# Optimization experiments

Measured on AMD Instinct MI355X. Metric: run time of the kernel, lower is better.

Reference implementation:

```python
import jax, jax.numpy as jnp
import numpy as np

N, E, B = 10000, 160000, 16
IN, H, A, L, OUT = 16, 64, 8, 2, 1
MSG_IN = 2 * (H + 1) + 1   # 131 = concat(x_i, x_j, additional_message_features)
UPD_IN = H + 1 + H         # 129 = concat(x_aug, aggregated message)


def _tp(h, a, W, b):
    # scalar-irreps fully-connected O3 tensor product == bilinear map + bias
    return jnp.einsum('ni,nj,ijk->nk', h, a, W) + b


def setup_inputs() -> dict:
    key = jax.random.key(0)
    ks = jax.random.split(key, 24)
    f32 = jnp.float32
    def rn(k, shape, scale=1.0):
        return jax.random.normal(k, shape, f32) * scale
    def w(k, shape):
        fan = shape[-3] * shape[-2]
        return rn(k, shape, 1.0 / np.sqrt(fan))
    return {
        'x': rn(ks[0], (N, IN)),
        'edge_index': jax.random.randint(ks[1], (2, E), 0, N),
        'edge_attr': rn(ks[2], (E, A)),
        'node_attr': rn(ks[3], (N, A)),
        'additional_message_features': rn(ks[4], (E, 1)),
        'additional_node_features': rn(ks[5], (N, 1)),
        'batch': jnp.sort(jax.random.randint(ks[6], (N,), 0, B)),
        'W_emb': w(ks[7], (IN + 1, A, H)), 'b_emb': jnp.zeros((H,), f32),
        'Wm1': w(ks[8], (L, MSG_IN, A, H)), 'bm1': jnp.zeros((L, H), f32),
        'Wm2': w(ks[9], (L, H, A, H)), 'bm2': jnp.zeros((L, H), f32),
        'Wu1': w(ks[10], (L, UPD_IN, A, H)), 'bu1': jnp.zeros((L, H), f32),
        'Wu2': w(ks[11], (L, H, A, H)), 'bu2': jnp.zeros((L, H), f32),
        'Wp1': w(ks[12], (H, A, H)), 'bp1': jnp.zeros((H,), f32),
        'Wp2': w(ks[13], (H, A, H)), 'bp2': jnp.zeros((H,), f32),
        'Wq1': rn(ks[14], (H, H), 1.0 / np.sqrt(H)), 'bq1': jnp.zeros((H,), f32),
        'Wq2': rn(ks[15], (H, OUT), 1.0 / np.sqrt(H)), 'bq2': jnp.zeros((OUT,), f32),
    }


def _forward(x, edge_attr, node_attr, amf, anf,
             W_emb, b_emb, Wm1, bm1, Wm2, bm2, Wu1, bu1, Wu2, bu2,
             Wp1, bp1, Wp2, bp2, Wq1, bq1, Wq2, bq2, edge_index, batch):
    silu = jax.nn.silu
    src, dst = edge_index[0], edge_index[1]  # source_to_target: aggregate at dst
    n = x.shape[0]
    # embedding: concat additional node features, bilinear TP with node_attr
    h = _tp(jnp.concatenate([x, anf], -1), node_attr, W_emb, b_emb)          # [N,H]
    for l in range(Wm1.shape[0]):  # loop over structurally distinct layers
        h_aug = jnp.concatenate([h, anf], -1)                                # [N,H+1]
        m_in = jnp.concatenate([h_aug[dst], h_aug[src], amf], -1)            # [E,MSG_IN]
        m = silu(_tp(m_in, edge_attr, Wm1[l], bm1[l]))                       # TP + swish gate
        m = silu(_tp(m, edge_attr, Wm2[l], bm2[l]))                          # sg2=True -> gated too
        agg = jax.ops.segment_sum(m, dst, num_segments=n)                    # scatter-add [N,H]
        u = silu(_tp(jnp.concatenate([h_aug, agg], -1), node_attr, Wu1[l], bu1[l]))
        u = _tp(u, node_attr, Wu2[l], bu2[l])                                # no gate on 2nd TP
        h = h + u                                                            # residual, adnid stripped
    # pre-pool MLP (SwishGate TP then plain TP)
    p = silu(_tp(h, node_attr, Wp1, bp1))
    p = _tp(p, node_attr, Wp2, bp2)                                          # [N,POOL=H]
    # global mean pool over graphs
    counts = jax.ops.segment_sum(jnp.ones((n,), p.dtype), batch, num_segments=B)
    g = jax.ops.segment_sum(p, batch, num_segments=B) / jnp.maximum(counts, 1.0)[:, None]
    # post-pool: TP with trivial 1x0e attr == plain linear
    g = silu(g @ Wq1 + bq1)
    return g @ Wq2 + bq2                                                     # [B,OUT]


def reference(x, edge_index, edge_attr, node_attr, additional_message_features,
              additional_node_features, batch, W_emb, b_emb, Wm1, bm1, Wm2, bm2,
              Wu1, bu1, Wu2, bu2, Wp1, bp1, Wp2, bp2, Wq1, bq1, Wq2, bq2):
    return _forward(x, edge_attr, node_attr, additional_message_features,
                    additional_node_features, W_emb, b_emb, Wm1, bm1, Wm2, bm2,
                    Wu1, bu1, Wu2, bu2, Wp1, bp1, Wp2, bp2, Wq1, bq1, Wq2, bq2,
                    edge_index, batch)
```

## Files before the change

kernel.cpp:

```cpp
#include <hip/hip_runtime.h>
#include <hip/hip_bf16.h>
#include <math.h>

constexpr int N = 10000;
constexpr int E = 160000;
constexpr int B = 16;
constexpr int POOL_CHUNKS = 80;
constexpr int MS = 72;
constexpr int HS = 96;

typedef short bf16x8 __attribute__((ext_vector_type(8)));
typedef short bf16x4 __attribute__((ext_vector_type(4)));
typedef float f32x4 __attribute__((ext_vector_type(4)));

__device__ __forceinline__ float silu_f(float x) {
    return x / (1.0f + __expf(-x));
}
__device__ __forceinline__ float bf2f(short s) {
    union { unsigned u; float f; } c; c.u = (unsigned)(unsigned short)s << 16; return c.f;
}

__global__ __launch_bounds__(256) void k_w2(
        const float* __restrict__ Wsrc,
        __hip_bfloat16* __restrict__ Whi, __hip_bfloat16* __restrict__ Wlo) {
    int idx = blockIdx.x * 256 + threadIdx.x;
    int l = idx >> 15;
    int rem = idx & 32767;
    int kk = rem >> 11;
    int nt = (rem >> 9) & 3;
    int c  = (rem >> 5) & 15;
    int q  = (rem >> 3) & 3;
    int j  = rem & 7;
    int i = q * 16 + kk;
    int k = nt * 16 + c;
    float wv = Wsrc[(size_t)l * 32768 + i * 512 + j * 64 + k];
    __hip_bfloat16 hi = __float2bfloat16(wv);
    Whi[idx] = hi;
    Wlo[idx] = __float2bfloat16(wv - __bfloat162float(hi));
}

__global__ __launch_bounds__(256) void k_w2h(
        const float* __restrict__ Wsrc, __hip_bfloat16* __restrict__ Whi) {
    int idx = blockIdx.x * 256 + threadIdx.x;
    int l = idx >> 15;
    int rem = idx & 32767;
    int kk = rem >> 11;
    int nt = (rem >> 9) & 3;
    int c  = (rem >> 5) & 15;
    int q  = (rem >> 3) & 3;
    int j  = rem & 7;
    int i = q * 16 + kk;
    int k = nt * 16 + c;
    Whi[idx] = __float2bfloat16(Wsrc[(size_t)l * 32768 + i * 512 + j * 64 + k]);
}

__global__ __launch_bounds__(256) void k_wu1(
        const float* __restrict__ Wu1,
        __hip_bfloat16* __restrict__ Whi, __hip_bfloat16* __restrict__ Wlo) {
    int idx = blockIdx.x * 256 + threadIdx.x;
    int l = idx / 67584;
    int rem = idx % 67584;
    int kk = rem / 2048;
    int r2 = rem % 2048;
    int nt = (r2 >> 9) & 3;
    int c  = (r2 >> 5) & 15;
    int q  = (r2 >> 3) & 3;
    int j  = r2 & 7;
    int i = q * 33 + kk;
    float wv = (i < 129) ? Wu1[(size_t)l * 129 * 512 + i * 512 + j * 64 + nt * 16 + c] : 0.f;
    __hip_bfloat16 hi = __float2bfloat16(wv);
    Whi[idx] = hi;
    Wlo[idx] = __float2bfloat16(wv - __bfloat162float(hi));
}

__global__ __launch_bounds__(256) void k_wm1z(
        const float* __restrict__ Wm1, __hip_bfloat16* __restrict__ Whi) {
    int idx = blockIdx.x * 256 + threadIdx.x;
    int l = idx / 71680;
    int rem = idx % 71680;
    int kkn = rem >> 9;
    int off = rem & 511;
    int kk = kkn >> 2;
    int nt = kkn & 3;
    int c16 = off >> 5;
    int q = (off >> 3) & 3;
    int j = off & 7;
    int k = nt * 16 + c16;
    int wi = -1;
    if (kk < 17) { int i = q * 17 + kk; if (i <= 64) wi = i; }
    else if (kk < 34) { int s = q * 17 + (kk - 17); if (s <= 64) wi = 65 + s; }
    else { if (q == 0) wi = 130; }
    float wv = (wi >= 0) ? Wm1[((size_t)l * 131 + wi) * 512 + j * 64 + k] : 0.f;
    Whi[idx] = __float2bfloat16(wv);
}

__device__ __forceinline__ void zgemm_stage(
        const __hip_bfloat16* xsrc, int xstride, int kkmax, int Lq,
        int w, int c16, int q, int lofs, const float* naA,
        const __hip_bfloat16* __restrict__ Whi, const __hip_bfloat16* __restrict__ Wlo,
        float (*part_s)[16][64]) {
    f32x4 zero4 = {0.f, 0.f, 0.f, 0.f};
    f32x4 acc[4];
#pragma unroll
    for (int nt = 0; nt < 4; ++nt) acc[nt] = zero4;
    for (int kk = w; kk < kkmax; kk += 4) {
        bf16x8 bh[4], bl[4];
#pragma unroll
        for (int nt = 0; nt < 4; ++nt) {
            int off = (kk * 4 + nt) * 512 + lofs;
            bh[nt] = *(const bf16x8*)(Whi + off);
            bl[nt] = *(const bf16x8*)(Wlo + off);
        }
        float mv = __bfloat162float(xsrc[c16 * xstride + q * Lq + kk]);
        union { bf16x8 v; __hip_bfloat16 hx[8]; } au;
#pragma unroll
        for (int j = 0; j < 8; ++j) au.hx[j] = __float2bfloat16(mv * naA[j]);
#pragma unroll
        for (int nt = 0; nt < 4; ++nt) {
            acc[nt] = __builtin_amdgcn_mfma_f32_16x16x32_bf16(au.v, bh[nt], acc[nt], 0, 0, 0);
            acc[nt] = __builtin_amdgcn_mfma_f32_16x16x32_bf16(au.v, bl[nt], acc[nt], 0, 0, 0);
        }
    }
#pragma unroll
    for (int nt = 0; nt < 4; ++nt)
#pragma unroll
        for (int r = 0; r < 4; ++r) part_s[w][q * 4 + r][nt * 16 + c16] = acc[nt][r];
}

__global__ __launch_bounds__(256) void k_embed_hb(
        const float* __restrict__ x, const float* __restrict__ anf,
        const float* __restrict__ na, const float* __restrict__ W_emb,
        const float* __restrict__ b_emb,
        float* __restrict__ h, __hip_bfloat16* __restrict__ hb, float* __restrict__ agg) {
    __shared__ float xs[16][18];
    __shared__ float na_s[16][8];
    int tid = threadIdx.x, w = tid >> 6, l = tid & 63;
    int n0 = blockIdx.x * 16;
    {
        int r = tid >> 4, c = tid & 15;
        xs[r][c] = x[(size_t)(n0 + r) * 16 + c];
    }
    if (tid < 16) xs[tid][16] = anf[n0 + tid];
    if (tid < 128) na_s[tid >> 3][tid & 7] = na[(size_t)n0 * 8 + tid];
    float4 z4 = {0.f, 0.f, 0.f, 0.f};
    ((float4*)(agg + (size_t)blockIdx.x * 1024))[tid] = z4;
    for (int t = tid; t < 192; t += 256)
        ((float4*)(hb + (size_t)n0 * HS))[t] = z4;
    __syncthreads();
    float acc[4];
#pragma unroll
    for (int t = 0; t < 4; ++t) acc[t] = b_emb[l];
    for (int i = 0; i < 17; ++i) {
#pragma unroll
        for (int j = 0; j < 8; ++j) {
            float wv = W_emb[(i * 8 + j) * 64 + l];
#pragma unroll
            for (int t = 0; t < 4; ++t) {
                int nn = w * 4 + t;
                acc[t] = fmaf(xs[nn][i] * na_s[nn][j], wv, acc[t]);
            }
        }
    }
    int slot = (l / 17) * 24 + l % 17;
#pragma unroll
    for (int t = 0; t < 4; ++t) {
        int n = n0 + w * 4 + t;
        h[(size_t)n * 64 + l] = acc[t];
        hb[(size_t)n * HS + slot] = __float2bfloat16(acc[t]);
    }
    if (tid < 16) hb[(size_t)(n0 + tid) * HS + 85] = __float2bfloat16(xs[tid][16]);
}

__global__ __launch_bounds__(256, 4) void k_edge(
        const int* __restrict__ eidx, const float* __restrict__ ea,
        const float* __restrict__ amf, const __hip_bfloat16* __restrict__ hb,
        const __hip_bfloat16* __restrict__ W1hi, const float* __restrict__ bm1_l,
        const __hip_bfloat16* __restrict__ W2hi,
        const float* __restrict__ bm2_l, float* __restrict__ agg) {
    __shared__ __align__(16) __hip_bfloat16 m_s[128 * MS];
    __shared__ float ea_s[128][9];
    __shared__ float amf_s[128];
    __shared__ int src_s[128], dst_s[128];
    __shared__ float bm1_s[64], bm2_s[64];
    int tid = threadIdx.x;
    int l = tid & 63, w = tid >> 6;
    int e0 = blockIdx.x * 128;
    for (int idx = tid; idx < 128; idx += 256) {
        src_s[idx] = eidx[e0 + idx];
        dst_s[idx] = eidx[E + e0 + idx];
        amf_s[idx] = amf[e0 + idx];
    }
    for (int idx = tid; idx < 1024; idx += 256) ea_s[idx >> 3][idx & 7] = ea[(size_t)e0 * 8 + idx];
    if (tid < 64) { bm1_s[tid] = bm1_l[tid]; bm2_s[tid] = bm2_l[tid]; }
    __syncthreads();

    int c16 = l & 15, q = l >> 4;
    int e0w = w * 32;
    float eaA[2][8];
    float amfA[2];
#pragma unroll
    for (int mt = 0; mt < 2; ++mt) {
#pragma unroll
        for (int j = 0; j < 8; ++j) eaA[mt][j] = ea_s[e0w + mt * 16 + c16][j];
        amfA[mt] = amf_s[e0w + mt * 16 + c16];
    }
    int lofs = (c16 * 4 + q) * 8;
    f32x4 zero4 = {0.f, 0.f, 0.f, 0.f};

    bf16x4 xD[2][5], xS[2][5];
#pragma unroll
    for (int mt = 0; mt < 2; ++mt) {
        const __hip_bfloat16* bd = hb + (size_t)dst_s[e0w + mt * 16 + c16] * HS + q * 24;
        const __hip_bfloat16* bs = hb + (size_t)src_s[e0w + mt * 16 + c16] * HS + q * 24;
#pragma unroll
        for (int t = 0; t < 5; ++t) {
            xD[mt][t] = *(const bf16x4*)(bd + t * 4);
            xS[mt][t] = *(const bf16x4*)(bs + t * 4);
        }
    }

    f32x4 acc1[2][4];
#pragma unroll
    for (int mt = 0; mt < 2; ++mt)
#pragma unroll
        for (int nt = 0; nt < 4; ++nt) acc1[mt][nt] = zero4;
#pragma unroll
    for (int kk = 0; kk < 17; ++kk) {
        bf16x8 bh[4];
#pragma unroll
        for (int nt = 0; nt < 4; ++nt)
            bh[nt] = *(const bf16x8*)(W1hi + (kk * 4 + nt) * 512 + lofs);
#pragma unroll
        for (int mt = 0; mt < 2; ++mt) {
            float xv = bf2f(xD[mt][kk >> 2][kk & 3]);
            union { bf16x8 v; __hip_bfloat16 hx[8]; } au;
#pragma unroll
            for (int j = 0; j < 8; ++j) au.hx[j] = __float2bfloat16(xv * eaA[mt][j]);
#pragma unroll
            for (int nt = 0; nt < 4; ++nt)
                acc1[mt][nt] = __builtin_amdgcn_mfma_f32_16x16x32_bf16(au.v, bh[nt], acc1[mt][nt], 0, 0, 0);
        }
    }
#pragma unroll
    for (int kk = 0; kk < 17; ++kk) {
        bf16x8 bh[4];
#pragma unroll
        for (int nt = 0; nt < 4; ++nt)
            bh[nt] = *(const bf16x8*)(W1hi + ((17 + kk) * 4 + nt) * 512 + lofs);
#pragma unroll
        for (int mt = 0; mt < 2; ++mt) {
            float xv = bf2f(xS[mt][kk >> 2][kk & 3]);
            union { bf16x8 v; __hip_bfloat16 hx[8]; } au;
#pragma unroll
            for (int j = 0; j < 8; ++j) au.hx[j] = __float2bfloat16(xv * eaA[mt][j]);
#pragma unroll
            for (int nt = 0; nt < 4; ++nt)
                acc1[mt][nt] = __builtin_amdgcn_mfma_f32_16x16x32_bf16(au.v, bh[nt], acc1[mt][nt], 0, 0, 0);
        }
    }
    {
        bf16x8 bh[4];
#pragma unroll
        for (int nt = 0; nt < 4; ++nt)
            bh[nt] = *(const bf16x8*)(W1hi + (34 * 4 + nt) * 512 + lofs);
#pragma unroll
        for (int mt = 0; mt < 2; ++mt) {
            float xv = (q == 0) ? amfA[mt] : 0.f;
            union { bf16x8 v; __hip_bfloat16 hx[8]; } au;
#pragma unroll
            for (int j = 0; j < 8; ++j) au.hx[j] = __float2bfloat16(xv * eaA[mt][j]);
#pragma unroll
            for (int nt = 0; nt < 4; ++nt)
                acc1[mt][nt] = __builtin_amdgcn_mfma_f32_16x16x32_bf16(au.v, bh[nt], acc1[mt][nt], 0, 0, 0);
        }
    }
#pragma unroll
    for (int mt = 0; mt < 2; ++mt)
#pragma unroll
        for (int nt = 0; nt < 4; ++nt) {
            int kd = nt * 16 + c16;
            float bias = bm1_s[kd];
#pragma unroll
            for (int r = 0; r < 4; ++r) {
                int e = e0w + mt * 16 + q * 4 + r;
                m_s[e * MS + kd] = __float2bfloat16(silu_f(bias + acc1[mt][nt][r]));
            }
        }

    bf16x4 mR[2][4];
#pragma unroll
    for (int mt = 0; mt < 2; ++mt)
#pragma unroll
        for (int t = 0; t < 4; ++t)
            mR[mt][t] = *(const bf16x4*)&m_s[(e0w + mt * 16 + c16) * MS + q * 16 + t * 4];

    f32x4 acc[2][4];
#pragma unroll
    for (int mt = 0; mt < 2; ++mt)
#pragma unroll
        for (int nt = 0; nt < 4; ++nt) acc[mt][nt] = zero4;
#pragma unroll
    for (int kk = 0; kk < 16; ++kk) {
        bf16x8 bh[4];
#pragma unroll
        for (int nt = 0; nt < 4; ++nt)
            bh[nt] = *(const bf16x8*)(W2hi + (kk * 4 + nt) * 512 + lofs);
#pragma unroll
        for (int mt = 0; mt < 2; ++mt) {
            float mv = bf2f(mR[mt][kk >> 2][kk & 3]);
            union { bf16x8 v; __hip_bfloat16 h[8]; } au;
#pragma unroll
            for (int j = 0; j < 8; ++j) au.h[j] = __float2bfloat16(mv * eaA[mt][j]);
#pragma unroll
            for (int nt = 0; nt < 4; ++nt)
                acc[mt][nt] = __builtin_amdgcn_mfma_f32_16x16x32_bf16(au.v, bh[nt], acc[mt][nt], 0, 0, 0);
        }
    }
#pragma unroll
    for (int mt = 0; mt < 2; ++mt)
#pragma unroll
        for (int nt = 0; nt < 4; ++nt) {
            int kd = nt * 16 + c16;
            float bias = bm2_s[kd];
#pragma unroll
            for (int r = 0; r < 4; ++r) {
                int e = e0w + mt * 16 + q * 4 + r;
                float v = silu_f(bias + acc[mt][nt][r]);
                atomicAdd(&agg[(size_t)dst_s[e] * 64 + kd], v);
            }
        }
}

__global__ __launch_bounds__(256) void k_upd_hb(
        const float* __restrict__ h_in, const float* __restrict__ anf,
        const float* __restrict__ na, const float* __restrict__ agg_in,
        const __hip_bfloat16* __restrict__ W1hi, const __hip_bfloat16* __restrict__ W1lo,
        const float* __restrict__ bu1_l,
        const __hip_bfloat16* __restrict__ W2hi_, const __hip_bfloat16* __restrict__ W2lo_,
        const float* __restrict__ bu2_l,
        float* __restrict__ h, __hip_bfloat16* __restrict__ hb, float* __restrict__ agg) {
    __shared__ __align__(16) __hip_bfloat16 xa_s[16 * 136];
    __shared__ __align__(16) __hip_bfloat16 u1_s[16 * 72];
    __shared__ float part_s[4][16][64];
    int tid = threadIdx.x;
    int w = tid >> 6, l = tid & 63;
    int n0 = blockIdx.x * 16;
    for (int idx = tid; idx < 16 * 132; idx += 256) {
        int r = idx / 132, c = idx % 132;
        int n = n0 + r;
        float v;
        if (c < 64) v = h_in[(size_t)n * 64 + c];
        else if (c == 64) v = anf[n];
        else if (c < 129) v = agg_in[(size_t)n * 64 + (c - 65)];
        else v = 0.f;
        xa_s[r * 136 + c] = __float2bfloat16(v);
    }
    int c16 = l & 15, q = l >> 4;
    float naA[8];
#pragma unroll
    for (int j = 0; j < 8; ++j) naA[j] = na[(size_t)(n0 + c16) * 8 + j];
    __syncthreads();
    float4 z4 = {0.f, 0.f, 0.f, 0.f};
    ((float4*)(agg + (size_t)blockIdx.x * 1024))[tid] = z4;
    for (int t = tid; t < 192; t += 256)
        ((float4*)(hb + (size_t)n0 * HS))[t] = z4;
    int lofs = (c16 * 4 + q) * 8;
    zgemm_stage(xa_s, 136, 33, 33, w, c16, q, lofs, naA, W1hi, W1lo, part_s);
    __syncthreads();
    for (int t = tid; t < 1024; t += 256) {
        int row = t >> 6, col = t & 63;
        float v = part_s[0][row][col] + part_s[1][row][col] + part_s[2][row][col] +
                  part_s[3][row][col] + bu1_l[col];
        u1_s[row * 72 + col] = __float2bfloat16(silu_f(v));
    }
    __syncthreads();
    zgemm_stage(u1_s, 72, 16, 16, w, c16, q, lofs, naA, W2hi_, W2lo_, part_s);
    __syncthreads();
    for (int t = tid; t < 1024; t += 256) {
        int row = t >> 6, col = t & 63;
        float v = part_s[0][row][col] + part_s[1][row][col] + part_s[2][row][col] +
                  part_s[3][row][col] + bu2_l[col];
        int n = n0 + row;
        float hn = h[(size_t)n * 64 + col] + v;
        h[(size_t)n * 64 + col] = hn;
        hb[(size_t)n * HS + (col / 17) * 24 + col % 17] = __float2bfloat16(hn);
    }
    if (tid < 16) hb[(size_t)(n0 + tid) * HS + 85] = __float2bfloat16(anf[n0 + tid]);
}

__global__ __launch_bounds__(256) void k_upd_prepool(
        const float* __restrict__ h_in, const float* __restrict__ anf,
        const float* __restrict__ na, const float* __restrict__ agg_in,
        const __hip_bfloat16* __restrict__ W1hi, const __hip_bfloat16* __restrict__ W1lo,
        const float* __restrict__ bu1_l,
        const __hip_bfloat16* __restrict__ W2hi_, const __hip_bfloat16* __restrict__ W2lo_,
        const float* __restrict__ bu2_l,
        const __hip_bfloat16* __restrict__ Wp1hi, const __hip_bfloat16* __restrict__ Wp1lo,
        const float* __restrict__ bp1,
        const __hip_bfloat16* __restrict__ Wp2hi, const __hip_bfloat16* __restrict__ Wp2lo,
        const float* __restrict__ bp2,
        float* __restrict__ p2) {
    __shared__ __align__(16) __hip_bfloat16 xa_s[16 * 136];
    __shared__ __align__(16) __hip_bfloat16 u1_s[16 * 72];
    __shared__ __align__(16) __hip_bfloat16 x2_s[16 * 72];
    __shared__ float part_s[4][16][64];
    int tid = threadIdx.x;
    int w = tid >> 6, l = tid & 63;
    int n0 = blockIdx.x * 16;
    for (int idx = tid; idx < 16 * 132; idx += 256) {
        int r = idx / 132, c = idx % 132;
        int n = n0 + r;
        float v;
        if (c < 64) v = h_in[(size_t)n * 64 + c];
        else if (c == 64) v = anf[n];
        else if (c < 129) v = agg_in[(size_t)n * 64 + (c - 65)];
        else v = 0.f;
        xa_s[r * 136 + c] = __float2bfloat16(v);
    }
    int c16 = l & 15, q = l >> 4;
    float naA[8];
#pragma unroll
    for (int j = 0; j < 8; ++j) naA[j] = na[(size_t)(n0 + c16) * 8 + j];
    __syncthreads();
    int lofs = (c16 * 4 + q) * 8;
    zgemm_stage(xa_s, 136, 33, 33, w, c16, q, lofs, naA, W1hi, W1lo, part_s);
    __syncthreads();
    for (int t = tid; t < 1024; t += 256) {
        int row = t >> 6, col = t & 63;
        float v = part_s[0][row][col] + part_s[1][row][col] + part_s[2][row][col] +
                  part_s[3][row][col] + bu1_l[col];
        u1_s[row * 72 + col] = __float2bfloat16(silu_f(v));
    }
    __syncthreads();
    zgemm_stage(u1_s, 72, 16, 16, w, c16, q, lofs, naA, W2hi_, W2lo_, part_s);
    __syncthreads();
    for (int t = tid; t < 1024; t += 256) {
        int row = t >> 6, col = t & 63;
        float v = part_s[0][row][col] + part_s[1][row][col] + part_s[2][row][col] +
                  part_s[3][row][col] + bu2_l[col];
        float hn = h_in[(size_t)(n0 + row) * 64 + col] + v;
        x2_s[row * 72 + col] = __float2bfloat16(hn);
    }
    __syncthreads();
    zgemm_stage(x2_s, 72, 16, 16, w, c16, q, lofs, naA, Wp1hi, Wp1lo, part_s);
    __syncthreads();
    for (int t = tid; t < 1024; t += 256) {
        int row = t >> 6, col = t & 63;
        float v = part_s[0][row][col] + part_s[1][row][col] + part_s[2][row][col] +
                  part_s[3][row][col] + bp1[col];
        u1_s[row * 72 + col] = __float2bfloat16(silu_f(v));
    }
    __syncthreads();
    zgemm_stage(u1_s, 72, 16, 16, w, c16, q, lofs, naA, Wp2hi, Wp2lo, part_s);
    __syncthreads();
    for (int t = tid; t < 1024; t += 256) {
        int row = t >> 6, col = t & 63;
        float v = part_s[0][row][col] + part_s[1][row][col] + part_s[2][row][col] +
                  part_s[3][row][col] + bp2[col];
        p2[(size_t)(n0 + row) * 64 + col] = v;
    }
}

__global__ __launch_bounds__(256) void k_pool(
        const float* __restrict__ p2, const int* __restrict__ batch,
        float* __restrict__ partial_p, float* __restrict__ partial_cnt) {
    __shared__ float acc_s[16 * 64];
    __shared__ float cnt_s[16];
    int tid = threadIdx.x;
    for (int idx = tid; idx < 1024; idx += 256) acc_s[idx] = 0.f;
    if (tid < 16) cnt_s[tid] = 0.f;
    __syncthreads();
    int w = tid >> 6, k = tid & 63;
    int base = blockIdx.x * 125;
    for (int i = 0; i < 32; ++i) {
        int nl = i * 4 + w;
        if (nl < 125) {
            int n = base + nl;
            int b = batch[n];
            atomicAdd(&acc_s[b * 64 + k], p2[(size_t)n * 64 + k]);
            if (k == 0) atomicAdd(&cnt_s[b], 1.0f);
        }
    }
    __syncthreads();
    for (int idx = tid; idx < 1024; idx += 256)
        partial_p[(size_t)blockIdx.x * 1024 + idx] = acc_s[idx];
    if (tid < 16) partial_cnt[blockIdx.x * 16 + tid] = cnt_s[tid];
}

__global__ __launch_bounds__(1024) void k_final(
        const float* __restrict__ partial_p, const float* __restrict__ partial_cnt,
        const float* __restrict__ Wq1, const float* __restrict__ bq1,
        const float* __restrict__ Wq2, const float* __restrict__ bq2,
        float* __restrict__ out) {
    __shared__ float g[16][64];
    int b = threadIdx.x >> 6, k = threadIdx.x & 63;
    float s = 0.f, cc = 0.f;
    for (int c = 0; c < POOL_CHUNKS; ++c) s += partial_p[(size_t)c * 1024 + b * 64 + k];
    for (int c = 0; c < POOL_CHUNKS; ++c) cc += partial_cnt[c * 16 + b];
    g[b][k] = s / fmaxf(cc, 1.0f);
    __syncthreads();
    float acc = bq1[k];
#pragma unroll
    for (int i = 0; i < 64; ++i) acc = fmaf(g[b][i], Wq1[i * 64 + k], acc);
    float v = silu_f(acc) * Wq2[k];
#pragma unroll
    for (int off = 32; off > 0; off >>= 1) v += __shfl_down(v, off, 64);
    if (k == 0) out[b] = v + bq2[0];
}

extern "C" void kernel_launch(void* const* d_in, const int* in_sizes, int n_in,
                              void* d_out, int out_size, void* d_ws, size_t ws_size,
                              hipStream_t stream) {
    const float* x    = (const float*)d_in[0];
    const int*   eidx = (const int*)  d_in[1];
    const float* ea   = (const float*)d_in[2];
    const float* na   = (const float*)d_in[3];
    const float* amf  = (const float*)d_in[4];
    const float* anf  = (const float*)d_in[5];
    const int*   batch= (const int*)  d_in[6];
    const float* W_emb= (const float*)d_in[7];
    const float* b_emb= (const float*)d_in[8];
    const float* Wm1  = (const float*)d_in[9];
    const float* bm1  = (const float*)d_in[10];
    const float* Wm2  = (const float*)d_in[11];
    const float* bm2  = (const float*)d_in[12];
    const float* Wu1  = (const float*)d_in[13];
    const float* bu1  = (const float*)d_in[14];
    const float* Wu2  = (const float*)d_in[15];
    const float* bu2  = (const float*)d_in[16];
    const float* Wp1  = (const float*)d_in[17];
    const float* bp1  = (const float*)d_in[18];
    const float* Wp2  = (const float*)d_in[19];
    const float* bp2  = (const float*)d_in[20];
    const float* Wq1  = (const float*)d_in[21];
    const float* bq1  = (const float*)d_in[22];
    const float* Wq2  = (const float*)d_in[23];
    const float* bq2  = (const float*)d_in[24];

    float* ws = (float*)d_ws;
    float* h      = ws;
    float* agg    = h + (size_t)N * 64;
    float* p2     = agg + (size_t)N * 64;
    float* part_p = p2 + (size_t)N * 64;
    float* part_c = part_p + POOL_CHUNKS * 1024;
    float* fend   = part_c + POOL_CHUNKS * 16;
    __hip_bfloat16* hb     = (__hip_bfloat16*)fend;
    __hip_bfloat16* W2hi   = hb + (size_t)N * HS;
    __hip_bfloat16* Wm1zhi = W2hi + 65536;
    __hip_bfloat16* Wu1hi  = Wm1zhi + 143360;
    __hip_bfloat16* Wu1lo  = Wu1hi + 135168;
    __hip_bfloat16* Wu2hi  = Wu1lo + 135168;
    __hip_bfloat16* Wu2lo  = Wu2hi + 65536;
    __hip_bfloat16* Wp1hi  = Wu2lo + 65536;
    __hip_bfloat16* Wp1lo  = Wp1hi + 32768;
    __hip_bfloat16* Wp2hi  = Wp1lo + 32768;
    __hip_bfloat16* Wp2lo  = Wp2hi + 32768;

    k_w2h<<<256, 256, 0, stream>>>(Wm2, W2hi);
    k_wm1z<<<560, 256, 0, stream>>>(Wm1, Wm1zhi);
    k_wu1<<<528, 256, 0, stream>>>(Wu1, Wu1hi, Wu1lo);
    k_w2<<<256, 256, 0, stream>>>(Wu2, Wu2hi, Wu2lo);
    k_w2<<<128, 256, 0, stream>>>(Wp1, Wp1hi, Wp1lo);
    k_w2<<<128, 256, 0, stream>>>(Wp2, Wp2hi, Wp2lo);

    k_embed_hb<<<625, 256, 0, stream>>>(x, anf, na, W_emb, b_emb, h, hb, agg);
    k_edge<<<E / 128, 256, 0, stream>>>(eidx, ea, amf, hb,
                                        Wm1zhi, bm1, W2hi, bm2, agg);
    k_upd_hb<<<625, 256, 0, stream>>>(h, anf, na, agg,
                                      Wu1hi, Wu1lo, bu1,
                                      Wu2hi, Wu2lo, bu2,
                                      h, hb, agg);
    k_edge<<<E / 128, 256, 0, stream>>>(eidx, ea, amf, hb,
                                        Wm1zhi + 71680, bm1 + 64,
                                        W2hi + 32768, bm2 + 64, agg);
    k_upd_prepool<<<625, 256, 0, stream>>>(h, anf, na, agg,
                                           Wu1hi + 67584, Wu1lo + 67584, bu1 + 64,
                                           Wu2hi + 32768, Wu2lo + 32768, bu2 + 64,
                                           Wp1hi, Wp1lo, bp1, Wp2hi, Wp2lo, bp2, p2);
    k_pool<<<POOL_CHUNKS, 256, 0, stream>>>(p2, batch, part_p, part_c);
    k_final<<<1, 1024, 0, stream>>>(part_p, part_c, Wq1, bq1, Wq2, bq2, (float*)d_out);
}
```

Baseline: 384.1 us.

## Sort edges by destination and reduce messages per segment before atomics

```diff
diff --git a/kernel.cpp b/kernel.cpp
--- a/kernel.cpp
+++ b/kernel.cpp
@@ -94,6 +94,61 @@
     Whi[idx] = __float2bfloat16(wv);
 }
 
+__global__ __launch_bounds__(256) void k_zero_i(int* __restrict__ p, int n) {
+    int i = blockIdx.x * 256 + threadIdx.x;
+    if (i < n) p[i] = 0;
+}
+
+__global__ __launch_bounds__(256) void k_hist(
+        const int* __restrict__ eidx, int* __restrict__ hist) {
+    int e = blockIdx.x * 256 + threadIdx.x;
+    if (e < E) atomicAdd(&hist[eidx[E + e]], 1);
+}
+
+__global__ __launch_bounds__(1024) void k_scan(
+        const int* __restrict__ hist, int* __restrict__ cursor) {
+    __shared__ int wsum[16];
+    int t = threadIdx.x;
+    int base = t * 10;
+    int loc[10];
+    int s = 0;
+#pragma unroll
+    for (int i = 0; i < 10; ++i) {
+        int v = (base + i < N) ? hist[base + i] : 0;
+        loc[i] = s;
+        s += v;
+    }
+    int lane = t & 63, w = t >> 6;
+    int incl = s;
+    for (int off = 1; off < 64; off <<= 1) {
+        int u = __shfl_up(incl, off, 64);
+        if (lane >= off) incl += u;
+    }
+    if (lane == 63) wsum[w] = incl;
+    __syncthreads();
+    if (t == 0) {
+        int a = 0;
+        for (int i2 = 0; i2 < 16; ++i2) { int v = wsum[i2]; wsum[i2] = a; a += v; }
+    }
+    __syncthreads();
+    int excl = incl - s + wsum[w];
+#pragma unroll
+    for (int i = 0; i < 10; ++i) {
+        int p = base + i;
+        if (p < N) cursor[p] = excl + loc[i];
+    }
+}
+
+__global__ __launch_bounds__(256) void k_scatter(
+        const int* __restrict__ eidx, int* __restrict__ cursor, int* __restrict__ perm) {
+    int e = blockIdx.x * 256 + threadIdx.x;
+    if (e < E) {
+        int d = eidx[E + e];
+        int p = atomicAdd(&cursor[d], 1);
+        perm[p] = e;
+    }
+}
+
 __device__ __forceinline__ void zgemm_stage(
         const __hip_bfloat16* xsrc, int xstride, int kkmax, int Lq,
         int w, int c16, int q, int lofs, const float* naA,
@@ -173,24 +228,32 @@
 
 __global__ __launch_bounds__(256, 4) void k_edge(
         const int* __restrict__ eidx, const float* __restrict__ ea,
-        const float* __restrict__ amf, const __hip_bfloat16* __restrict__ hb,
+        const float* __restrict__ amf, const int* __restrict__ perm,
+        const __hip_bfloat16* __restrict__ hb,
         const __hip_bfloat16* __restrict__ W1hi, const float* __restrict__ bm1_l,
         const __hip_bfloat16* __restrict__ W2hi,
         const float* __restrict__ bm2_l, float* __restrict__ agg) {
-    __shared__ __align__(16) __hip_bfloat16 m_s[128 * MS];
-    __shared__ float ea_s[128][9];
+    __shared__ __align__(16) char smem_u[128 * 66 * 4];
     __shared__ float amf_s[128];
     __shared__ int src_s[128], dst_s[128];
     __shared__ float bm1_s[64], bm2_s[64];
+    float* ea_s = (float*)smem_u;
+    __hip_bfloat16* m_s = (__hip_bfloat16*)(smem_u + 4608);
+    float* m2 = (float*)smem_u;
+
     int tid = threadIdx.x;
     int l = tid & 63, w = tid >> 6;
     int e0 = blockIdx.x * 128;
     for (int idx = tid; idx < 128; idx += 256) {
-        src_s[idx] = eidx[e0 + idx];
-        dst_s[idx] = eidx[E + e0 + idx];
-        amf_s[idx] = amf[e0 + idx];
-    }
-    for (int idx = tid; idx < 1024; idx += 256) ea_s[idx >> 3][idx & 7] = ea[(size_t)e0 * 8 + idx];
+        int pe = perm[e0 + idx];
+        src_s[idx] = eidx[pe];
+        dst_s[idx] = eidx[E + pe];
+        amf_s[idx] = amf[pe];
+    }
+    for (int idx = tid; idx < 1024; idx += 256) {
+        int pe = perm[e0 + (idx >> 3)];
+        ea_s[(idx >> 3) * 9 + (idx & 7)] = ea[(size_t)pe * 8 + (idx & 7)];
+    }
     if (tid < 64) { bm1_s[tid] = bm1_l[tid]; bm2_s[tid] = bm2_l[tid]; }
     __syncthreads();
 
@@ -201,7 +264,7 @@
 #pragma unroll
     for (int mt = 0; mt < 2; ++mt) {
 #pragma unroll
-        for (int j = 0; j < 8; ++j) eaA[mt][j] = ea_s[e0w + mt * 16 + c16][j];
+        for (int j = 0; j < 8; ++j) eaA[mt][j] = ea_s[(e0w + mt * 16 + c16) * 9 + j];
         amfA[mt] = amf_s[e0w + mt * 16 + c16];
     }
     int lofs = (c16 * 4 + q) * 8;
@@ -294,6 +357,8 @@
         for (int t = 0; t < 4; ++t)
             mR[mt][t] = *(const bf16x4*)&m_s[(e0w + mt * 16 + c16) * MS + q * 16 + t * 4];
 
+    __syncthreads();
+
     f32x4 acc[2][4];
 #pragma unroll
     for (int mt = 0; mt < 2; ++mt)
@@ -325,10 +390,25 @@
 #pragma unroll
             for (int r = 0; r < 4; ++r) {
                 int e = e0w + mt * 16 + q * 4 + r;
-                float v = silu_f(bias + acc[mt][nt][r]);
-                atomicAdd(&agg[(size_t)dst_s[e] * 64 + kd], v);
+                m2[e * 66 + kd] = silu_f(bias + acc[mt][nt][r]);
             }
         }
+
+    {
+        int r0 = w * 32;
+        float run = 0.f;
+        int cur_d = dst_s[r0];
+        for (int e = r0; e < r0 + 32; ++e) {
+            int d = dst_s[e];
+            if (d != cur_d) {
+                atomicAdd(&agg[(size_t)cur_d * 64 + l], run);
+                run = 0.f;
+                cur_d = d;
+            }
+            run += m2[e * 66 + l];
+        }
+        atomicAdd(&agg[(size_t)cur_d * 64 + l], run);
+    }
 }
 
 __global__ __launch_bounds__(256) void k_upd_hb(
@@ -555,6 +635,14 @@
     __hip_bfloat16* Wp1lo  = Wp1hi + 32768;
     __hip_bfloat16* Wp2hi  = Wp1lo + 32768;
     __hip_bfloat16* Wp2lo  = Wp2hi + 32768;
+    int* hist   = (int*)(Wp2lo + 32768);
+    int* cursor = hist + N;
+    int* perm   = cursor + N;
+
+    k_zero_i<<<(N + 255) / 256, 256, 0, stream>>>(hist, N);
+    k_hist<<<(E + 255) / 256, 256, 0, stream>>>(eidx, hist);
+    k_scan<<<1, 1024, 0, stream>>>(hist, cursor);
+    k_scatter<<<(E + 255) / 256, 256, 0, stream>>>(eidx, cursor, perm);
 
     k_w2h<<<256, 256, 0, stream>>>(Wm2, W2hi);
     k_wm1z<<<560, 256, 0, stream>>>(Wm1, Wm1zhi);
@@ -564,13 +652,13 @@
     k_w2<<<128, 256, 0, stream>>>(Wp2, Wp2hi, Wp2lo);
 
     k_embed_hb<<<625, 256, 0, stream>>>(x, anf, na, W_emb, b_emb, h, hb, agg);
-    k_edge<<<E / 128, 256, 0, stream>>>(eidx, ea, amf, hb,
+    k_edge<<<E / 128, 256, 0, stream>>>(eidx, ea, amf, perm, hb,
                                         Wm1zhi, bm1, W2hi, bm2, agg);
     k_upd_hb<<<625, 256, 0, stream>>>(h, anf, na, agg,
                                       Wu1hi, Wu1lo, bu1,
                                       Wu2hi, Wu2lo, bu2,
                                       h, hb, agg);
-    k_edge<<<E / 128, 256, 0, stream>>>(eidx, ea, amf, hb,
+    k_edge<<<E / 128, 256, 0, stream>>>(eidx, ea, amf, perm, hb,
                                         Wm1zhi + 71680, bm1 + 64,
                                         W2hi + 32768, bm2 + 64, agg);
     k_upd_prepool<<<625, 256, 0, stream>>>(h, anf, na, agg,
```

Result: slower. 392.5 us (+2.2%).
